# Kernel tuning notes

Measured on AMD Instinct MI355X. Metric: run time of the kernel, lower is better.

## Reference

```python
import jax, jax.numpy as jnp
import numpy as np
from jax import lax

V, E, H = 32000, 256, 512
B, S, T = 32, 512, 30
BOS = 1


def gru_cell(x, h, w_ih, w_hh, b_ih, b_hh):
    # PyTorch GRU cell math. x: [B,E_in], h: [B,H]
    gi = x @ w_ih.T + b_ih            # [B,3H]
    gh = h @ w_hh.T + b_hh            # [B,3H]
    i_r, i_z, i_n = jnp.split(gi, 3, axis=-1)
    h_r, h_z, h_n = jnp.split(gh, 3, axis=-1)
    r = jax.nn.sigmoid(i_r + h_r)
    z = jax.nn.sigmoid(i_z + h_z)
    n = jnp.tanh(i_n + r * h_n)
    return (1.0 - z) * n + z * h


def setup_inputs() -> dict:
    key = jax.random.key(0)
    ks = jax.random.split(key, 18)
    f = lambda k, shape: (jax.random.normal(k, shape, jnp.float32) * 0.05)
    return {
        "body": jax.random.randint(ks[0], (B, S), 0, V, dtype=jnp.int32),
        "max_new_tokens": T,
        "enc_emb": f(ks[1], (V, E)),
        "enc_wih_f": f(ks[2], (3 * H, E)),
        "enc_whh_f": f(ks[3], (3 * H, H)),
        "enc_bih_f": f(ks[4], (3 * H,)),
        "enc_bhh_f": f(ks[5], (3 * H,)),
        "enc_wih_b": f(ks[6], (3 * H, E)),
        "enc_whh_b": f(ks[7], (3 * H, H)),
        "enc_bih_b": f(ks[8], (3 * H,)),
        "enc_bhh_b": f(ks[9], (3 * H,)),
        "dec_emb": f(ks[10], (V, E)),
        "dec_wih": f(ks[11], (3 * H, E)),
        "dec_whh": f(ks[12], (3 * H, H)),
        "dec_bih": f(ks[13], (3 * H,)),
        "dec_bhh": f(ks[14], (3 * H,)),
        "fc_w": f(ks[15], (V, H)),
        "fc_b": f(ks[16], (V,)),
    }


def reference(body, max_new_tokens, enc_emb, enc_wih_f, enc_whh_f, enc_bih_f,
              enc_bhh_f, enc_wih_b, enc_whh_b, enc_bih_b, enc_bhh_b,
              dec_emb, dec_wih, dec_whh, dec_bih, dec_bhh, fc_w, fc_b):
    batch = body.shape[0]
    hdim = enc_whh_f.shape[1]

    # ----- Encoder: bidirectional GRU, sum of final fwd/bwd hidden states -----
    emb = enc_emb[body]                     # [B,S,E] (dropout = identity in eval)
    xs = jnp.swapaxes(emb, 0, 1)            # [S,B,E]
    h0 = jnp.zeros((batch, hdim), emb.dtype)

    def step_f(h, x):
        return gru_cell(x, h, enc_wih_f, enc_whh_f, enc_bih_f, enc_bhh_f), None

    def step_b(h, x):
        return gru_cell(x, h, enc_wih_b, enc_whh_b, enc_bih_b, enc_bhh_b), None

    h_fwd, _ = lax.scan(step_f, h0, xs)
    h_bwd, _ = lax.scan(step_b, h0, xs[::-1])
    hidden = h_fwd + h_bwd                  # [B,H]  (== hidden[0] + hidden[1])

    tok0 = jnp.full((batch,), BOS, dtype=jnp.int32)

    def dec_step(carry, _):
        h, tok = carry
        x = dec_emb[tok]                                    # [B,E]
        h = gru_cell(x, h, dec_wih, dec_whh, dec_bih, dec_bhh)
        logits = h @ fc_w.T + fc_b                          # [B,V]
        nxt = jnp.argmax(logits, axis=-1).astype(jnp.int32)
        return (h, nxt), logits

    _, logits_seq = lax.scan(dec_step, (hidden, tok0), None,
                             length=max_new_tokens)          # [T,B,V]
    return jnp.swapaxes(logits_seq, 0, 1)                    # [B,T,V]
```

## Files before the change

### kernel.cpp

```cpp
#include <hip/hip_runtime.h>
#include <math.h>

#define BB 32
#define SS 512
#define EE 256
#define HH 512
#define VV 32000
#define TT 30
#define WPH 516

typedef unsigned long long ull;

__device__ __forceinline__ float4 ldf4(const float* p) {
    return *reinterpret_cast<const float4*>(p);
}
__device__ __forceinline__ float sigmoidf_(float x) {
    return 1.0f / (1.0f + expf(-x));
}
__device__ __forceinline__ void fma4(float4& a, float s, const float4& b) {
    a.x = fmaf(s, b.x, a.x); a.y = fmaf(s, b.y, a.y);
    a.z = fmaf(s, b.z, a.z); a.w = fmaf(s, b.w, a.w);
}
__device__ __forceinline__ ull mkkey(float val, int v) {
    unsigned u = __float_as_uint(val);
    u = (u >> 31) ? ~u : (u | 0x80000000u);
    return ((ull)u << 32) | (0xFFFFFFFFu - (unsigned)v);
}
__device__ __forceinline__ ull sxmax(ull k, int m) {
    unsigned hi = (unsigned)(k >> 32), lo = (unsigned)k;
    unsigned oh = __shfl_xor(hi, m), ol = __shfl_xor(lo, m);
    ull o = ((ull)oh << 32) | ol;
    return o > k ? o : k;
}
__device__ __forceinline__ ull cld8(const ull* p) {
    return __hip_atomic_load(p, __ATOMIC_RELAXED, __HIP_MEMORY_SCOPE_AGENT);
}
__device__ __forceinline__ void cst4(float* p, float v) {
    __hip_atomic_store(p, v, __ATOMIC_RELAXED, __HIP_MEMORY_SCOPE_AGENT);
}

__device__ __forceinline__ void gbar(unsigned* fl, int me, int n, int tid,
                                     unsigned tgt) {
    __syncthreads();
    if (tid == 0)
        __hip_atomic_store(fl + (size_t)me * 32, tgt, __ATOMIC_RELEASE,
                           __HIP_MEMORY_SCOPE_AGENT);
    if (tid < n) {
        while (__hip_atomic_load(fl + (size_t)tid * 32, __ATOMIC_RELAXED,
                                 __HIP_MEMORY_SCOPE_AGENT) < tgt)
            __builtin_amdgcn_s_sleep(2);
    }
    __syncthreads();
}

#define GATE4(acc0, acc1, W, h00, h01, h10, h11, h20, h21, h30, h31) \
    fma4(acc0, W.x, h00); fma4(acc1, W.x, h01);                      \
    fma4(acc0, W.y, h10); fma4(acc1, W.y, h11);                      \
    fma4(acc0, W.z, h20); fma4(acc1, W.z, h21);                      \
    fma4(acc0, W.w, h30); fma4(acc1, W.w, h31);

#define XR4(vv, m) { vv.x += __shfl_xor(vv.x, m); vv.y += __shfl_xor(vv.y, m); \
                     vv.z += __shfl_xor(vv.z, m); vv.w += __shfl_xor(vv.w, m); }

__global__ __launch_bounds__(256, 1) void enc_persist3(
    const int* __restrict__ body,
    const float* __restrict__ enc_emb,
    const float* __restrict__ wih_f, const float* __restrict__ whh_f,
    const float* __restrict__ bih_f, const float* __restrict__ bhh_f,
    const float* __restrict__ wih_b, const float* __restrict__ whh_b,
    const float* __restrict__ bih_b, const float* __restrict__ bhh_b,
    float* __restrict__ hD,
    unsigned* __restrict__ flagE)
{
    const int bid = blockIdx.x;
    const int tid = threadIdx.x;
    const int d   = bid & 7;
    const int m   = bid >> 3;
    const int dir = d >> 2;
    const int bg  = d & 3;
    const int jc  = m;

    const float* wih = dir ? wih_b : wih_f;
    const float* whh = dir ? whh_b : whh_f;
    const float* bih = dir ? bih_b : bih_f;
    const float* bhh = dir ? bhh_b : bhh_f;

    __shared__ float wlds[16 * 3 * WPH];
    __shared__ float hlds[512 * 8];
    __shared__ float xlds[256 * 8];
    __shared__ float part[2][16][33];
    __shared__ float blds[16][4];

    for (int idx = tid; idx < 48 * 128; idx += 256) {
        const int row = idx >> 7;
        const int q   = idx & 127;
        const int jl0 = row / 3, g = row - jl0 * 3;
        const int k   = q * 4;
        float4 v = ldf4(whh + (size_t)(g * HH + jc * 16 + jl0) * HH + k);
        float* dst = wlds + row * WPH + k;
        dst[0] = v.x; dst[1] = v.y; dst[2] = v.z; dst[3] = v.w;
    }
    if (tid < 16) {
        const int jg = jc * 16 + tid;
        blds[tid][0] = bih[jg] + bhh[jg];
        blds[tid][1] = bih[jg + HH] + bhh[jg + HH];
        blds[tid][2] = bih[jg + 2 * HH];
        blds[tid][3] = bhh[jg + 2 * HH];
    }

    const int ks   = tid >> 4;
    const int jl   = tid & 15;
    const int jg   = jc * 16 + jl;
    const int lane = tid & 63;
    const int wv   = tid >> 6;
    const float* wj = wlds + (jl * 3) * WPH;
    const float* wr_i = wih + (size_t)jg            * EE;
    const float* wz_i = wih + (size_t)(jg + HH)     * EE;
    const float* wn_i = wih + (size_t)(jg + 2 * HH) * EE;
    float* hdom = hD + (size_t)d * 2 * 4096;
    unsigned* fdom = flagE + (size_t)d * 1024;

    for (int t = 0; t < SS; ++t) {
        const int p = t & 1;

        {
            const ull* hsU = (const ull*)(hdom + p * 4096);
            ull hv[8];
            #pragma unroll
            for (int i = 0; i < 8; ++i) hv[i] = cld8(hsU + tid * 8 + i);
            ull* hlU = (ull*)hlds;
            #pragma unroll
            for (int i = 0; i < 8; ++i) hlU[tid * 8 + i] = hv[i];
        }
        {
            const int sb = tid & 7, kc = tid >> 3;
            const int s = dir ? (SS - 1 - t) : t;
            const int tk = body[(bg * 8 + sb) * SS + s];
            const float* xr = enc_emb + (size_t)tk * EE + kc * 8;
            float4 v0 = ldf4(xr), v1 = ldf4(xr + 4);
            const int k0 = kc * 8;
            xlds[(k0 + 0) * 8 + sb] = v0.x; xlds[(k0 + 1) * 8 + sb] = v0.y;
            xlds[(k0 + 2) * 8 + sb] = v0.z; xlds[(k0 + 3) * 8 + sb] = v0.w;
            xlds[(k0 + 4) * 8 + sb] = v1.x; xlds[(k0 + 5) * 8 + sb] = v1.y;
            xlds[(k0 + 6) * 8 + sb] = v1.z; xlds[(k0 + 7) * 8 + sb] = v1.w;
        }
        __syncthreads();

        float4 aR0 = {0,0,0,0}, aR1 = {0,0,0,0};
        float4 aZ0 = {0,0,0,0}, aZ1 = {0,0,0,0};
        float4 aN0 = {0,0,0,0}, aN1 = {0,0,0,0};
        float4 aI0 = {0,0,0,0}, aI1 = {0,0,0,0};

        #pragma unroll
        for (int q = 0; q < 8; ++q) {
            const int k = ks * 32 + q * 4;
            float4 wr = ldf4(wj + 0 * WPH + k);
            float4 wz = ldf4(wj + 1 * WPH + k);
            float4 wn = ldf4(wj + 2 * WPH + k);
            const float* hk = hlds + k * 8;
            float4 h00 = ldf4(hk +  0), h01 = ldf4(hk +  4);
            float4 h10 = ldf4(hk +  8), h11 = ldf4(hk + 12);
            float4 h20 = ldf4(hk + 16), h21 = ldf4(hk + 20);
            float4 h30 = ldf4(hk + 24), h31 = ldf4(hk + 28);
            GATE4(aR0, aR1, wr, h00, h01, h10, h11, h20, h21, h30, h31);
            GATE4(aZ0, aZ1, wz, h00, h01, h10, h11, h20, h21, h30, h31);
            GATE4(aN0, aN1, wn, h00, h01, h10, h11, h20, h21, h30, h31);
        }
        #pragma unroll
        for (int q = 0; q < 4; ++q) {
            const int k = ks * 16 + q * 4;
            float4 wr = ldf4(wr_i + k);
            float4 wz = ldf4(wz_i + k);
            float4 wn = ldf4(wn_i + k);
            const float* xk = xlds + k * 8;
            float4 x00 = ldf4(xk +  0), x01 = ldf4(xk +  4);
            float4 x10 = ldf4(xk +  8), x11 = ldf4(xk + 12);
            float4 x20 = ldf4(xk + 16), x21 = ldf4(xk + 20);
            float4 x30 = ldf4(xk + 24), x31 = ldf4(xk + 28);
            GATE4(aR0, aR1, wr, x00, x01, x10, x11, x20, x21, x30, x31);
            GATE4(aZ0, aZ1, wz, x00, x01, x10, x11, x20, x21, x30, x31);
            GATE4(aI0, aI1, wn, x00, x01, x10, x11, x20, x21, x30, x31);
        }

        XR4(aR0, 16); XR4(aR0, 32); XR4(aR1, 16); XR4(aR1, 32);
        XR4(aZ0, 16); XR4(aZ0, 32); XR4(aZ1, 16); XR4(aZ1, 32);
        XR4(aN0, 16); XR4(aN0, 32); XR4(aN1, 16); XR4(aN1, 32);
        XR4(aI0, 16); XR4(aI0, 32); XR4(aI1, 16); XR4(aI1, 32);

        if (wv < 2 && (lane >> 4) == 0) {
            float* pr = &part[wv][jl][0];
            pr[ 0]=aR0.x; pr[ 1]=aR0.y; pr[ 2]=aR0.z; pr[ 3]=aR0.w;
            pr[ 4]=aR1.x; pr[ 5]=aR1.y; pr[ 6]=aR1.z; pr[ 7]=aR1.w;
            pr[ 8]=aZ0.x; pr[ 9]=aZ0.y; pr[10]=aZ0.z; pr[11]=aZ0.w;
            pr[12]=aZ1.x; pr[13]=aZ1.y; pr[14]=aZ1.z; pr[15]=aZ1.w;
            pr[16]=aN0.x; pr[17]=aN0.y; pr[18]=aN0.z; pr[19]=aN0.w;
            pr[20]=aN1.x; pr[21]=aN1.y; pr[22]=aN1.z; pr[23]=aN1.w;
            pr[24]=aI0.x; pr[25]=aI0.y; pr[26]=aI0.z; pr[27]=aI0.w;
            pr[28]=aI1.x; pr[29]=aI1.y; pr[30]=aI1.z; pr[31]=aI1.w;
        }
        __syncthreads();
        if (wv >= 2 && (lane >> 4) == 0) {
            float* pr = &part[wv - 2][jl][0];
            pr[ 0]+=aR0.x; pr[ 1]+=aR0.y; pr[ 2]+=aR0.z; pr[ 3]+=aR0.w;
            pr[ 4]+=aR1.x; pr[ 5]+=aR1.y; pr[ 6]+=aR1.z; pr[ 7]+=aR1.w;
            pr[ 8]+=aZ0.x; pr[ 9]+=aZ0.y; pr[10]+=aZ0.z; pr[11]+=aZ0.w;
            pr[12]+=aZ1.x; pr[13]+=aZ1.y; pr[14]+=aZ1.z; pr[15]+=aZ1.w;
            pr[16]+=aN0.x; pr[17]+=aN0.y; pr[18]+=aN0.z; pr[19]+=aN0.w;
            pr[20]+=aN1.x; pr[21]+=aN1.y; pr[22]+=aN1.z; pr[23]+=aN1.w;
            pr[24]+=aI0.x; pr[25]+=aI0.y; pr[26]+=aI0.z; pr[27]+=aI0.w;
            pr[28]+=aI1.x; pr[29]+=aI1.y; pr[30]+=aI1.z; pr[31]+=aI1.w;
        }
        __syncthreads();

        if (tid < 128) {
            const int j2 = tid >> 3, b = tid & 7;
            float sR = part[0][j2][b]      + part[1][j2][b]      + blds[j2][0];
            float sZ = part[0][j2][8 + b]  + part[1][j2][8 + b]  + blds[j2][1];
            float sN = part[0][j2][16 + b] + part[1][j2][16 + b] + blds[j2][3];
            float sI = part[0][j2][24 + b] + part[1][j2][24 + b] + blds[j2][2];
            const float r = sigmoidf_(sR);
            const float z = sigmoidf_(sZ);
            const float n = tanhf(sI + r * sN);
            const int jw = jc * 16 + j2;
            const float hold = hlds[jw * 8 + b];
            cst4(hdom + (p ^ 1) * 4096 + jw * 8 + b, (1.0f - z) * n + z * hold);
        }

        if (t < SS - 1)
            gbar(fdom, m, 32, tid, (unsigned)(t + 1));
        else
            __syncthreads();
    }
}

__global__ __launch_bounds__(256) void enc_fin(
    const float* __restrict__ hD, float* __restrict__ hdT)
{
    const int i = blockIdx.x * 256 + threadIdx.x;
    const int k = i >> 5, b = i & 31;
    const int bg = b >> 3, sb = b & 7;
    hdT[i] = hD[(size_t)bg * 8192 + k * 8 + sb]
           + hD[(size_t)(4 + bg) * 8192 + k * 8 + sb];
}

__global__ __launch_bounds__(1024, 4) void dec_persist3(
    const float* __restrict__ dec_emb,
    const float* __restrict__ wih, const float* __restrict__ whh,
    const float* __restrict__ bih, const float* __restrict__ bhh,
    const float* __restrict__ fc_w, const float* __restrict__ fc_b,
    const float* __restrict__ hdT,
    float* __restrict__ hdG,
    ull* __restrict__ cand,
    float* __restrict__ out,
    unsigned* __restrict__ flagD)
{
    const int bid = blockIdx.x;
    const int tid = threadIdx.x;

    __shared__ float hlds[512 * 32];
    __shared__ float xls[256 * 32];
    __shared__ float partD[16][64][4];
    __shared__ ull lwred[16][8][4];
    __shared__ ull candp[32][33];
    __shared__ int tokL[32];

    float bR = 0, bZ = 0, bI = 0, bN = 0;
    if (tid < 64) {
        const int j2 = bid * 2 + (tid & 1);
        bR = bih[j2] + bhh[j2];
        bZ = bih[j2 + HH] + bhh[j2 + HH];
        bI = bih[j2 + 2 * HH];
        bN = bhh[j2 + 2 * HH];
    }

    for (int i = tid; i < 4096; i += 1024) {
        *(float4*)(hlds + i * 4) = ldf4(hdT + i * 4);
    }

    for (int t = 0; t < TT; ++t) {
        if (t == 0) {
            if (tid < 32) tokL[tid] = 1;
        } else {
            {
                const int b = tid & 31, cc = tid >> 5;
                ull km = 0ull;
                #pragma unroll
                for (int i = 0; i < 8; ++i) {
                    ull k2 = cld8(cand + (size_t)(cc * 8 + i) * 32 + b);
                    if (k2 > km) km = k2;
                }
                candp[cc][b] = km;
            }
            __syncthreads();
            if (tid < 32) {
                ull m2 = candp[0][tid];
                for (int c2 = 1; c2 < 32; ++c2) {
                    ull k2 = candp[c2][tid];
                    if (k2 > m2) m2 = k2;
                }
                tokL[tid] = (int)(0xFFFFFFFFu - (unsigned)(m2 & 0xFFFFFFFFull));
            }
        }
        __syncthreads();

        {
            const int b = tid & 31, kc = tid >> 5;
            const float* xr = dec_emb + (size_t)tokL[b] * EE + kc * 8;
            float4 v0 = ldf4(xr), v1 = ldf4(xr + 4);
            const int k0 = kc * 8;
            xls[(k0 + 0) * 32 + b] = v0.x; xls[(k0 + 1) * 32 + b] = v0.y;
            xls[(k0 + 2) * 32 + b] = v0.z; xls[(k0 + 3) * 32 + b] = v0.w;
            xls[(k0 + 4) * 32 + b] = v1.x; xls[(k0 + 5) * 32 + b] = v1.y;
            xls[(k0 + 6) * 32 + b] = v1.z; xls[(k0 + 7) * 32 + b] = v1.w;
        }
        __syncthreads();

        {
            const int ks = tid >> 6, b = (tid >> 1) & 31, jl = tid & 1;
            const int j = bid * 2 + jl;
            float sR = 0.f, sZ = 0.f, sN = 0.f, sI = 0.f;
            const float* wr_h = whh + (size_t)j            * HH;
            const float* wz_h = whh + (size_t)(j + HH)     * HH;
            const float* wn_h = whh + (size_t)(j + 2 * HH) * HH;
            #pragma unroll
            for (int q = 0; q < 8; ++q) {
                const int k = ks * 32 + q * 4;
                float4 wr = ldf4(wr_h + k), wz = ldf4(wz_h + k), wn = ldf4(wn_h + k);
                float h0 = hlds[(k + 0) * 32 + b], h1 = hlds[(k + 1) * 32 + b];
                float h2 = hlds[(k + 2) * 32 + b], h3 = hlds[(k + 3) * 32 + b];
                sR = fmaf(wr.x, h0, fmaf(wr.y, h1, fmaf(wr.z, h2, fmaf(wr.w, h3, sR))));
                sZ = fmaf(wz.x, h0, fmaf(wz.y, h1, fmaf(wz.z, h2, fmaf(wz.w, h3, sZ))));
                sN = fmaf(wn.x, h0, fmaf(wn.y, h1, fmaf(wn.z, h2, fmaf(wn.w, h3, sN))));
            }
            const float* wr_x = wih + (size_t)j            * EE;
            const float* wz_x = wih + (size_t)(j + HH)     * EE;
            const float* wn_x = wih + (size_t)(j + 2 * HH) * EE;
            #pragma unroll
            for (int q = 0; q < 4; ++q) {
                const int k = ks * 16 + q * 4;
                float4 wr = ldf4(wr_x + k), wz = ldf4(wz_x + k), wn = ldf4(wn_x + k);
                float x0 = xls[(k + 0) * 32 + b], x1 = xls[(k + 1) * 32 + b];
                float x2 = xls[(k + 2) * 32 + b], x3 = xls[(k + 3) * 32 + b];
                sR = fmaf(wr.x, x0, fmaf(wr.y, x1, fmaf(wr.z, x2, fmaf(wr.w, x3, sR))));
                sZ = fmaf(wz.x, x0, fmaf(wz.y, x1, fmaf(wz.z, x2, fmaf(wz.w, x3, sZ))));
                sI = fmaf(wn.x, x0, fmaf(wn.y, x1, fmaf(wn.z, x2, fmaf(wn.w, x3, sI))));
            }
            float* pd = &partD[ks][b * 2 + jl][0];
            pd[0] = sR; pd[1] = sZ; pd[2] = sN; pd[3] = sI;
        }
        __syncthreads();
        if (tid < 64) {
            const int b = tid >> 1, jl = tid & 1;
            const int j = bid * 2 + jl;
            float sR = bR, sZ = bZ, sN = bN, sI = bI;
            #pragma unroll
            for (int q2 = 0; q2 < 16; ++q2) {
                sR += partD[q2][tid][0]; sZ += partD[q2][tid][1];
                sN += partD[q2][tid][2]; sI += partD[q2][tid][3];
            }
            const float r = sigmoidf_(sR);
            const float z = sigmoidf_(sZ);
            const float n = tanhf(sI + r * sN);
            const float hold = hlds[j * 32 + b];
            cst4(hdG + (size_t)j * 32 + b, (1.0f - z) * n + z * hold);
        }

        gbar(flagD, bid, 256, tid, (unsigned)(2 * t + 1));

        {
            const ull* hU = (const ull*)hdG;
            ull hv[8];
            #pragma unroll
            for (int i = 0; i < 8; ++i) hv[i] = cld8(hU + tid * 8 + i);
            ull* hlU = (ull*)hlds;
            #pragma unroll
            for (int i = 0; i < 8; ++i) hlU[tid * 8 + i] = hv[i];
        }
        __syncthreads();

        {
            const int wave = tid >> 6, lane = tid & 63;
            const int bh = lane & 7, ks = (lane >> 3) & 3, vh = lane >> 5;
            const int voff = wave * 8 + vh * 4;
            const int vb   = bid * 125;
            const int k0   = ks * 128;

            const int o0 = voff,     o1 = voff + 1;
            const int o2 = voff + 2, o3 = voff + 3;
            const int v0 = vb + (o0 < 125 ? o0 : 124);
            const int v1 = vb + (o1 < 125 ? o1 : 124);
            const int v2 = vb + (o2 < 125 ? o2 : 124);
            const int v3 = vb + (o3 < 125 ? o3 : 124);
            const float* w0p = fc_w + (size_t)v0 * HH;
            const float* w1p = fc_w + (size_t)v1 * HH;
            const float* w2p = fc_w + (size_t)v2 * HH;
            const float* w3p = fc_w + (size_t)v3 * HH;

            float4 acc0 = {0,0,0,0}, acc1 = {0,0,0,0};
            float4 acc2 = {0,0,0,0}, acc3 = {0,0,0,0};

            for (int kk = 0; kk < 128; kk += 4) {
                const int k = k0 + kk;
                float4 w0 = ldf4(w0p + k), w1 = ldf4(w1p + k);
                float4 w2 = ldf4(w2p + k), w3 = ldf4(w3p + k);
                const float* hb = hlds + k * 32 + bh * 4;
                float4 h0 = ldf4(hb), h1 = ldf4(hb + 32);
                float4 h2 = ldf4(hb + 64), h3 = ldf4(hb + 96);
                fma4(acc0, w0.x, h0); fma4(acc0, w0.y, h1); fma4(acc0, w0.z, h2); fma4(acc0, w0.w, h3);
                fma4(acc1, w1.x, h0); fma4(acc1, w1.y, h1); fma4(acc1, w1.z, h2); fma4(acc1, w1.w, h3);
                fma4(acc2, w2.x, h0); fma4(acc2, w2.y, h1); fma4(acc2, w2.z, h2); fma4(acc2, w2.w, h3);
                fma4(acc3, w3.x, h0); fma4(acc3, w3.y, h1); fma4(acc3, w3.z, h2); fma4(acc3, w3.w, h3);
            }
            XR4(acc0, 8); XR4(acc0, 16);
            XR4(acc1, 8); XR4(acc1, 16);
            XR4(acc2, 8); XR4(acc2, 16);
            XR4(acc3, 8); XR4(acc3, 16);

            const int b0 = bh * 4;
            ull kb0 = 0, kb1 = 0, kb2 = 0, kb3 = 0;
            #pragma unroll
            for (int i = 0; i < 4; ++i) {
                const int off = voff + i;
                if (off < 125) {
                    const int v = vb + off;
                    float4 a = (i == 0) ? acc0 : (i == 1) ? acc1
                             : (i == 2) ? acc2 : acc3;
                    const float fb = fc_b[v];
                    a.x += fb; a.y += fb; a.z += fb; a.w += fb;
                    if (ks == 0) {
                        out[((size_t)((b0 + 0) * TT + t)) * VV + v] = a.x;
                        out[((size_t)((b0 + 1) * TT + t)) * VV + v] = a.y;
                        out[((size_t)((b0 + 2) * TT + t)) * VV + v] = a.z;
                        out[((size_t)((b0 + 3) * TT + t)) * VV + v] = a.w;
                    }
                    ull t0 = mkkey(a.x, v); if (t0 > kb0) kb0 = t0;
                    ull t1 = mkkey(a.y, v); if (t1 > kb1) kb1 = t1;
                    ull t2 = mkkey(a.z, v); if (t2 > kb2) kb2 = t2;
                    ull t3 = mkkey(a.w, v); if (t3 > kb3) kb3 = t3;
                }
            }
            kb0 = sxmax(kb0, 32); kb1 = sxmax(kb1, 32);
            kb2 = sxmax(kb2, 32); kb3 = sxmax(kb3, 32);
            if (lane < 8) {
                lwred[wave][bh][0] = kb0; lwred[wave][bh][1] = kb1;
                lwred[wave][bh][2] = kb2; lwred[wave][bh][3] = kb3;
            }
        }
        __syncthreads();
        if (tid < 32) {
            ull km = lwred[0][tid >> 2][tid & 3];
            #pragma unroll
            for (int w2 = 1; w2 < 16; ++w2) {
                ull k2 = lwred[w2][tid >> 2][tid & 3];
                if (k2 > km) km = k2;
            }
            __hip_atomic_store(cand + (size_t)bid * 32 + tid, km,
                               __ATOMIC_RELAXED, __HIP_MEMORY_SCOPE_AGENT);
        }

        if (t < TT - 1)
            gbar(flagD, bid, 256, tid, (unsigned)(2 * t + 2));
    }
}

extern "C" void kernel_launch(void* const* d_in, const int* in_sizes, int n_in,
                              void* d_out, int out_size, void* d_ws, size_t ws_size,
                              hipStream_t stream) {
    (void)in_sizes; (void)n_in; (void)out_size; (void)ws_size;

    const int*   body    = (const int*)  d_in[0];
    const float* enc_emb = (const float*)d_in[2];
    const float* wih_f   = (const float*)d_in[3];
    const float* whh_f   = (const float*)d_in[4];
    const float* bih_f   = (const float*)d_in[5];
    const float* bhh_f   = (const float*)d_in[6];
    const float* wih_b   = (const float*)d_in[7];
    const float* whh_b   = (const float*)d_in[8];
    const float* bih_b   = (const float*)d_in[9];
    const float* bhh_b   = (const float*)d_in[10];
    const float* dec_emb = (const float*)d_in[11];
    const float* dwih    = (const float*)d_in[12];
    const float* dwhh    = (const float*)d_in[13];
    const float* dbih    = (const float*)d_in[14];
    const float* dbhh    = (const float*)d_in[15];
    const float* fc_w    = (const float*)d_in[16];
    const float* fc_b    = (const float*)d_in[17];
    float* out = (float*)d_out;

    char* ws = (char*)d_ws;
    float* hD    = (float*)(ws);
    float* hdT   = (float*)(ws + 262144);
    float* hdG   = (float*)(ws + 327680);
    ull*   cand  = (ull*)  (ws + 393216);
    unsigned* flagE = (unsigned*)(ws + 458752);
    unsigned* flagD = (unsigned*)(ws + 491520);

    (void)hipMemsetAsync(hD, 0, 262144, stream);
    (void)hipMemsetAsync(flagE, 0, 65536, stream);

    enc_persist3<<<256, 256, 0, stream>>>(
        body, enc_emb, wih_f, whh_f, bih_f, bhh_f,
        wih_b, whh_b, bih_b, bhh_b, hD, flagE);

    enc_fin<<<64, 256, 0, stream>>>(hD, hdT);

    dec_persist3<<<256, 1024, 0, stream>>>(
        dec_emb, dwih, dwhh, dbih, dbhh, fc_w, fc_b,
        hdT, hdG, cand, out, flagD);
}
```

Baseline: 6.290 ms.

## Pad shared-memory h/x tiles, batch fc_w loads, relax barrier release ordering

Adds padding to the encoder and decoder shared-memory tiles for hidden state and inputs so that ks-strided float4 reads fall in different LDS banks. The decoder's fc projection loop now loads 16 fc_w floats per row before doing the FMAs, giving more memory-level parallelism. The grid barrier flag store changes from release to relaxed and the spin sleep is shortened to lower barrier latency. The relaxed store may weaken the ordering between the cross-block h writes and the flag, which risks correctness.

```diff
diff --git a/kernel.cpp b/kernel.cpp
--- a/kernel.cpp
+++ b/kernel.cpp
@@ -38,17 +38,21 @@
 __device__ __forceinline__ void cst4(float* p, float v) {
     __hip_atomic_store(p, v, __ATOMIC_RELAXED, __HIP_MEMORY_SCOPE_AGENT);
 }
+__device__ __forceinline__ void xr4(float4& v, int m) {
+    v.x += __shfl_xor(v.x, m); v.y += __shfl_xor(v.y, m);
+    v.z += __shfl_xor(v.z, m); v.w += __shfl_xor(v.w, m);
+}
 
 __device__ __forceinline__ void gbar(unsigned* fl, int me, int n, int tid,
                                      unsigned tgt) {
     __syncthreads();
     if (tid == 0)
-        __hip_atomic_store(fl + (size_t)me * 32, tgt, __ATOMIC_RELEASE,
+        __hip_atomic_store(fl + (size_t)me * 32, tgt, __ATOMIC_RELAXED,
                            __HIP_MEMORY_SCOPE_AGENT);
     if (tid < n) {
         while (__hip_atomic_load(fl + (size_t)tid * 32, __ATOMIC_RELAXED,
                                  __HIP_MEMORY_SCOPE_AGENT) < tgt)
-            __builtin_amdgcn_s_sleep(2);
+            __builtin_amdgcn_s_sleep(1);
     }
     __syncthreads();
 }
@@ -59,10 +63,10 @@
     fma4(acc0, W.z, h20); fma4(acc1, W.z, h21);                      \
     fma4(acc0, W.w, h30); fma4(acc1, W.w, h31);
 
-#define XR4(vv, m) { vv.x += __shfl_xor(vv.x, m); vv.y += __shfl_xor(vv.y, m); \
-                     vv.z += __shfl_xor(vv.z, m); vv.w += __shfl_xor(vv.w, m); }
-
-__global__ __launch_bounds__(256, 1) void enc_persist3(
+#define FXE_H(k) ((k) * 8 + (((k) >> 5) << 2))
+#define FXE_X(k) ((k) * 8 + (((k) >> 4) << 2))
+
+__global__ __launch_bounds__(256, 1) void enc_persist5(
     const int* __restrict__ body,
     const float* __restrict__ enc_emb,
     const float* __restrict__ wih_f, const float* __restrict__ whh_f,
@@ -85,9 +89,9 @@
     const float* bih = dir ? bih_b : bih_f;
     const float* bhh = dir ? bhh_b : bhh_f;
 
-    __shared__ float wlds[16 * 3 * WPH];
-    __shared__ float hlds[512 * 8];
-    __shared__ float xlds[256 * 8];
+    __shared__ float wlds[48 * WPH];
+    __shared__ float hlds[4160];
+    __shared__ float xlds[2112];
     __shared__ float part[2][16][33];
     __shared__ float blds[16][4];
 
@@ -123,14 +127,11 @@
     for (int t = 0; t < SS; ++t) {
         const int p = t & 1;
 
+        ull hv[8];
         {
             const ull* hsU = (const ull*)(hdom + p * 4096);
-            ull hv[8];
             #pragma unroll
             for (int i = 0; i < 8; ++i) hv[i] = cld8(hsU + tid * 8 + i);
-            ull* hlU = (ull*)hlds;
-            #pragma unroll
-            for (int i = 0; i < 8; ++i) hlU[tid * 8 + i] = hv[i];
         }
         {
             const int sb = tid & 7, kc = tid >> 3;
@@ -138,11 +139,17 @@
             const int tk = body[(bg * 8 + sb) * SS + s];
             const float* xr = enc_emb + (size_t)tk * EE + kc * 8;
             float4 v0 = ldf4(xr), v1 = ldf4(xr + 4);
-            const int k0 = kc * 8;
-            xlds[(k0 + 0) * 8 + sb] = v0.x; xlds[(k0 + 1) * 8 + sb] = v0.y;
-            xlds[(k0 + 2) * 8 + sb] = v0.z; xlds[(k0 + 3) * 8 + sb] = v0.w;
-            xlds[(k0 + 4) * 8 + sb] = v1.x; xlds[(k0 + 5) * 8 + sb] = v1.y;
-            xlds[(k0 + 6) * 8 + sb] = v1.z; xlds[(k0 + 7) * 8 + sb] = v1.w;
+            const int base = kc * 64 + ((kc >> 1) << 2);
+            xlds[base +  0 + sb] = v0.x; xlds[base +  8 + sb] = v0.y;
+            xlds[base + 16 + sb] = v0.z; xlds[base + 24 + sb] = v0.w;
+            xlds[base + 32 + sb] = v1.x; xlds[base + 40 + sb] = v1.y;
+            xlds[base + 48 + sb] = v1.z; xlds[base + 56 + sb] = v1.w;
+        }
+        {
+            ull* hlU = (ull*)hlds;
+            const int base = tid * 8 + ((tid >> 4) << 1);
+            #pragma unroll
+            for (int i = 0; i < 8; ++i) hlU[base + i] = hv[i];
         }
         __syncthreads();
 
@@ -157,7 +164,7 @@
             float4 wr = ldf4(wj + 0 * WPH + k);
             float4 wz = ldf4(wj + 1 * WPH + k);
             float4 wn = ldf4(wj + 2 * WPH + k);
-            const float* hk = hlds + k * 8;
+            const float* hk = hlds + k * 8 + (ks << 2);
             float4 h00 = ldf4(hk +  0), h01 = ldf4(hk +  4);
             float4 h10 = ldf4(hk +  8), h11 = ldf4(hk + 12);
             float4 h20 = ldf4(hk + 16), h21 = ldf4(hk + 20);
@@ -172,7 +179,7 @@
             float4 wr = ldf4(wr_i + k);
             float4 wz = ldf4(wz_i + k);
             float4 wn = ldf4(wn_i + k);
-            const float* xk = xlds + k * 8;
+            const float* xk = xlds + k * 8 + (ks << 2);
             float4 x00 = ldf4(xk +  0), x01 = ldf4(xk +  4);
             float4 x10 = ldf4(xk +  8), x11 = ldf4(xk + 12);
             float4 x20 = ldf4(xk + 16), x21 = ldf4(xk + 20);
@@ -182,10 +189,10 @@
             GATE4(aI0, aI1, wn, x00, x01, x10, x11, x20, x21, x30, x31);
         }
 
-        XR4(aR0, 16); XR4(aR0, 32); XR4(aR1, 16); XR4(aR1, 32);
-        XR4(aZ0, 16); XR4(aZ0, 32); XR4(aZ1, 16); XR4(aZ1, 32);
-        XR4(aN0, 16); XR4(aN0, 32); XR4(aN1, 16); XR4(aN1, 32);
-        XR4(aI0, 16); XR4(aI0, 32); XR4(aI1, 16); XR4(aI1, 32);
+        xr4(aR0, 16); xr4(aR0, 32); xr4(aR1, 16); xr4(aR1, 32);
+        xr4(aZ0, 16); xr4(aZ0, 32); xr4(aZ1, 16); xr4(aZ1, 32);
+        xr4(aN0, 16); xr4(aN0, 32); xr4(aN1, 16); xr4(aN1, 32);
+        xr4(aI0, 16); xr4(aI0, 32); xr4(aI1, 16); xr4(aI1, 32);
 
         if (wv < 2 && (lane >> 4) == 0) {
             float* pr = &part[wv][jl][0];
@@ -222,7 +229,7 @@
             const float z = sigmoidf_(sZ);
             const float n = tanhf(sI + r * sN);
             const int jw = jc * 16 + j2;
-            const float hold = hlds[jw * 8 + b];
+            const float hold = hlds[FXE_H(jw) + b];
             cst4(hdom + (p ^ 1) * 4096 + jw * 8 + b, (1.0f - z) * n + z * hold);
         }
 
@@ -243,7 +250,9 @@
            + hD[(size_t)(4 + bg) * 8192 + k * 8 + sb];
 }
 
-__global__ __launch_bounds__(1024, 4) void dec_persist3(
+#define FXD(k) ((k) * 32 + (((k) >> 7) * 20))
+
+__global__ __launch_bounds__(1024, 4) void dec_persist5(
     const float* __restrict__ dec_emb,
     const float* __restrict__ wih, const float* __restrict__ whh,
     const float* __restrict__ bih, const float* __restrict__ bhh,
@@ -257,7 +266,7 @@
     const int bid = blockIdx.x;
     const int tid = threadIdx.x;
 
-    __shared__ float hlds[512 * 32];
+    __shared__ float hlds2[16464];
     __shared__ float xls[256 * 32];
     __shared__ float partD[16][64][4];
     __shared__ ull lwred[16][8][4];
@@ -274,7 +283,7 @@
     }
 
     for (int i = tid; i < 4096; i += 1024) {
-        *(float4*)(hlds + i * 4) = ldf4(hdT + i * 4);
+        *(float4*)(hlds2 + i * 4 + (i >> 10) * 20) = ldf4(hdT + i * 4);
     }
 
     for (int t = 0; t < TT; ++t) {
@@ -319,6 +328,7 @@
             const int ks = tid >> 6, b = (tid >> 1) & 31, jl = tid & 1;
             const int j = bid * 2 + jl;
             float sR = 0.f, sZ = 0.f, sN = 0.f, sI = 0.f;
+            const float* hpA = hlds2 + (size_t)ks * 1024 + (ks >> 2) * 20 + b;
             const float* wr_h = whh + (size_t)j            * HH;
             const float* wz_h = whh + (size_t)(j + HH)     * HH;
             const float* wn_h = whh + (size_t)(j + 2 * HH) * HH;
@@ -326,8 +336,8 @@
             for (int q = 0; q < 8; ++q) {
                 const int k = ks * 32 + q * 4;
                 float4 wr = ldf4(wr_h + k), wz = ldf4(wz_h + k), wn = ldf4(wn_h + k);
-                float h0 = hlds[(k + 0) * 32 + b], h1 = hlds[(k + 1) * 32 + b];
-                float h2 = hlds[(k + 2) * 32 + b], h3 = hlds[(k + 3) * 32 + b];
+                const float* hq = hpA + q * 128;
+                float h0 = hq[0], h1 = hq[32], h2 = hq[64], h3 = hq[96];
                 sR = fmaf(wr.x, h0, fmaf(wr.y, h1, fmaf(wr.z, h2, fmaf(wr.w, h3, sR))));
                 sZ = fmaf(wz.x, h0, fmaf(wz.y, h1, fmaf(wz.z, h2, fmaf(wz.w, h3, sZ))));
                 sN = fmaf(wn.x, h0, fmaf(wn.y, h1, fmaf(wn.z, h2, fmaf(wn.w, h3, sN))));
@@ -361,7 +371,7 @@
             const float r = sigmoidf_(sR);
             const float z = sigmoidf_(sZ);
             const float n = tanhf(sI + r * sN);
-            const float hold = hlds[j * 32 + b];
+            const float hold = hlds2[FXD(j) + b];
             cst4(hdG + (size_t)j * 32 + b, (1.0f - z) * n + z * hold);
         }
 
@@ -372,49 +382,63 @@
             ull hv[8];
             #pragma unroll
             for (int i = 0; i < 8; ++i) hv[i] = cld8(hU + tid * 8 + i);
-            ull* hlU = (ull*)hlds;
-            #pragma unroll
-            for (int i = 0; i < 8; ++i) hlU[tid * 8 + i] = hv[i];
-        }
-        __syncthreads();
-
-        {
-            const int wave = tid >> 6, lane = tid & 63;
+            const int k = tid >> 1, half = tid & 1;
+            ull* hlU = (ull*)hlds2;
+            const int base = k * 16 + (k >> 7) * 10 + half * 8;
+            #pragma unroll
+            for (int i = 0; i < 8; ++i) hlU[base + i] = hv[i];
+        }
+        __syncthreads();
+
+        {
+            const int lane = tid & 63, wavei = tid >> 6;
             const int bh = lane & 7, ks = (lane >> 3) & 3, vh = lane >> 5;
-            const int voff = wave * 8 + vh * 4;
-            const int vb   = bid * 125;
-            const int k0   = ks * 128;
-
-            const int o0 = voff,     o1 = voff + 1;
-            const int o2 = voff + 2, o3 = voff + 3;
-            const int v0 = vb + (o0 < 125 ? o0 : 124);
-            const int v1 = vb + (o1 < 125 ? o1 : 124);
-            const int v2 = vb + (o2 < 125 ? o2 : 124);
-            const int v3 = vb + (o3 < 125 ? o3 : 124);
-            const float* w0p = fc_w + (size_t)v0 * HH;
-            const float* w1p = fc_w + (size_t)v1 * HH;
-            const float* w2p = fc_w + (size_t)v2 * HH;
-            const float* w3p = fc_w + (size_t)v3 * HH;
+            const int voff = wavei * 8 + vh * 4;
+            const int vb = bid * 125;
+            const int k0 = ks * 128;
+
+            const int o0 = voff < 125 ? voff : 124;
+            const int o1 = voff + 1 < 125 ? voff + 1 : 124;
+            const int o2 = voff + 2 < 125 ? voff + 2 : 124;
+            const int o3 = voff + 3 < 125 ? voff + 3 : 124;
+            const float* wp0 = fc_w + (size_t)(vb + o0) * HH;
+            const float* wp1 = fc_w + (size_t)(vb + o1) * HH;
+            const float* wp2 = fc_w + (size_t)(vb + o2) * HH;
+            const float* wp3 = fc_w + (size_t)(vb + o3) * HH;
 
             float4 acc0 = {0,0,0,0}, acc1 = {0,0,0,0};
             float4 acc2 = {0,0,0,0}, acc3 = {0,0,0,0};
 
-            for (int kk = 0; kk < 128; kk += 4) {
+            for (int kk = 0; kk < 128; kk += 16) {
                 const int k = k0 + kk;
-                float4 w0 = ldf4(w0p + k), w1 = ldf4(w1p + k);
-                float4 w2 = ldf4(w2p + k), w3 = ldf4(w3p + k);
-                const float* hb = hlds + k * 32 + bh * 4;
-                float4 h0 = ldf4(hb), h1 = ldf4(hb + 32);
-                float4 h2 = ldf4(hb + 64), h3 = ldf4(hb + 96);
-                fma4(acc0, w0.x, h0); fma4(acc0, w0.y, h1); fma4(acc0, w0.z, h2); fma4(acc0, w0.w, h3);
-                fma4(acc1, w1.x, h0); fma4(acc1, w1.y, h1); fma4(acc1, w1.z, h2); fma4(acc1, w1.w, h3);
-                fma4(acc2, w2.x, h0); fma4(acc2, w2.y, h1); fma4(acc2, w2.z, h2); fma4(acc2, w2.w, h3);
-                fma4(acc3, w3.x, h0); fma4(acc3, w3.y, h1); fma4(acc3, w3.z, h2); fma4(acc3, w3.w, h3);
-            }
-            XR4(acc0, 8); XR4(acc0, 16);
-            XR4(acc1, 8); XR4(acc1, 16);
-            XR4(acc2, 8); XR4(acc2, 16);
-            XR4(acc3, 8); XR4(acc3, 16);
+                float4 wl0[4], wl1[4], wl2[4], wl3[4];
+                #pragma unroll
+                for (int q = 0; q < 4; ++q) {
+                    wl0[q] = ldf4(wp0 + k + q * 4);
+                    wl1[q] = ldf4(wp1 + k + q * 4);
+                    wl2[q] = ldf4(wp2 + k + q * 4);
+                    wl3[q] = ldf4(wp3 + k + q * 4);
+                }
+                #pragma unroll
+                for (int q = 0; q < 4; ++q) {
+                    const int kq = k + q * 4;
+                    const float* hq = hlds2 + kq * 32 + ((kq >> 7) * 20) + bh * 4;
+                    float4 h0 = ldf4(hq),      h1 = ldf4(hq + 32);
+                    float4 h2 = ldf4(hq + 64), h3 = ldf4(hq + 96);
+                    fma4(acc0, wl0[q].x, h0); fma4(acc0, wl0[q].y, h1);
+                    fma4(acc0, wl0[q].z, h2); fma4(acc0, wl0[q].w, h3);
+                    fma4(acc1, wl1[q].x, h0); fma4(acc1, wl1[q].y, h1);
+                    fma4(acc1, wl1[q].z, h2); fma4(acc1, wl1[q].w, h3);
+                    fma4(acc2, wl2[q].x, h0); fma4(acc2, wl2[q].y, h1);
+                    fma4(acc2, wl2[q].z, h2); fma4(acc2, wl2[q].w, h3);
+                    fma4(acc3, wl3[q].x, h0); fma4(acc3, wl3[q].y, h1);
+                    fma4(acc3, wl3[q].z, h2); fma4(acc3, wl3[q].w, h3);
+                }
+            }
+            xr4(acc0, 8); xr4(acc0, 16);
+            xr4(acc1, 8); xr4(acc1, 16);
+            xr4(acc2, 8); xr4(acc2, 16);
+            xr4(acc3, 8); xr4(acc3, 16);
 
             const int b0 = bh * 4;
             ull kb0 = 0, kb1 = 0, kb2 = 0, kb3 = 0;
@@ -442,8 +466,8 @@
             kb0 = sxmax(kb0, 32); kb1 = sxmax(kb1, 32);
             kb2 = sxmax(kb2, 32); kb3 = sxmax(kb3, 32);
             if (lane < 8) {
-                lwred[wave][bh][0] = kb0; lwred[wave][bh][1] = kb1;
-                lwred[wave][bh][2] = kb2; lwred[wave][bh][3] = kb3;
+                lwred[wavei][bh][0] = kb0; lwred[wavei][bh][1] = kb1;
+                lwred[wavei][bh][2] = kb2; lwred[wavei][bh][3] = kb3;
             }
         }
         __syncthreads();
@@ -498,13 +522,13 @@
     (void)hipMemsetAsync(hD, 0, 262144, stream);
     (void)hipMemsetAsync(flagE, 0, 65536, stream);
 
-    enc_persist3<<<256, 256, 0, stream>>>(
+    enc_persist5<<<256, 256, 0, stream>>>(
         body, enc_emb, wih_f, whh_f, bih_f, bhh_f,
         wih_b, whh_b, bih_b, bhh_b, hD, flagE);
 
     enc_fin<<<64, 256, 0, stream>>>(hD, hdT);
 
-    dec_persist3<<<256, 1024, 0, stream>>>(
+    dec_persist5<<<256, 1024, 0, stream>>>(
         dec_emb, dwih, dwhh, dbih, dbhh, fc_w, fc_b,
         hdT, hdG, cand, out, flagD);
 }
```

Measured after the change: 5.636 ms, median of 3. 1.12x faster.
